# Optimization experiments

Hardware: AMD Instinct MI355X
Metric: run time of the kernel (lower is better)

## Reference

```python
import jax, jax.numpy as jnp
import numpy as np

B, C2D, C3D, H, W, N = 4, 64, 64, 256, 256, 16384
NEG_SLOPE = 0.1


def _conv1x1_lrelu(x, w, b):
    # 1x1 conv (no norm) + leaky_relu(0.1), per Conv2dNormRelu defaults
    y = jnp.einsum('bchw,oc->bohw', x, w) + b[None, :, None, None]
    return jax.nn.leaky_relu(y, NEG_SLOPE)


def _batch_gather(feat, idx):
    # feat: [B, C, N], idx: [B, P] -> [B, C, P]
    return jnp.take_along_axis(feat, idx[:, None, :], axis=2)


def setup_inputs() -> dict:
    key = jax.random.key(0)
    ks = jax.random.split(key, 14)
    f = jax.random.normal
    s = 0.05
    return {
        'xy': jax.random.uniform(ks[0], (B, 2, N), jnp.float32) * jnp.float32(W),
        'feat_2d': f(ks[1], (B, C2D, H, W), jnp.float32),
        'feat_3d': f(ks[2], (B, C3D, N), jnp.float32),
        'last_flow_2d': f(ks[3], (B, 2, H, W), jnp.float32),
        'last_flow_3d_to_2d': f(ks[4], (B, 2, N), jnp.float32),
        'nn_proj': jax.random.randint(ks[5], (B, H, W, 1), 0, N, jnp.int32),
        'w1': f(ks[6], (C3D, C3D + 5), jnp.float32) * s,
        'b1': f(ks[7], (C3D,), jnp.float32) * s,
        'w2': f(ks[8], (C3D, C3D), jnp.float32) * s,
        'b2': f(ks[9], (C3D,), jnp.float32) * s,
        'w3': f(ks[10], (C3D, C3D), jnp.float32) * s,
        'b3': f(ks[11], (C3D,), jnp.float32) * s,
        'wf': f(ks[12], (C2D, C2D + C3D), jnp.float32) * s,
        'bf': f(ks[13], (C2D,), jnp.float32) * s,
    }


def reference(xy, feat_2d, feat_3d, last_flow_2d, last_flow_3d_to_2d, nn_proj,
              w1, b1, w2, b2, w3, b3, wf, bf):
    b, _, h, w = feat_2d.shape
    # concat per-point flow onto 3D features: [B, C3D+2, N]
    feat_3d_aug = jnp.concatenate([feat_3d, last_flow_3d_to_2d], axis=1)

    idx = nn_proj[..., 0].reshape(b, h * w)  # nearest-neighbor point per pixel
    gathered = _batch_gather(feat_3d_aug, idx).reshape(b, -1, h, w)  # [B, C3D+2, H, W]
    xy_proj = _batch_gather(xy, idx).reshape(b, 2, h, w)             # [B, 2, H, W]

    # pixel-coordinate mesh grid: channel 0 = x (width), channel 1 = y (height)
    gy, gx = jnp.meshgrid(jnp.arange(h, dtype=xy.dtype), jnp.arange(w, dtype=xy.dtype), indexing='ij')
    grid = jnp.stack([gx, gy], axis=0)[None]  # [1, 2, H, W]
    offset = xy_proj - grid                    # [B, 2, H, W]

    # correlation between gathered 3D feats and 2D feats (channel mean)
    corr = jnp.mean(gathered[:, :C2D] * feat_2d, axis=1, keepdims=True)  # [B, 1, H, W]

    # last 2 channels are the projected flow; subtract detached last_flow_2d
    flow_ch = gathered[:, -2:] - jax.lax.stop_gradient(last_flow_2d)
    x = jnp.concatenate([corr, offset, gathered[:, :-2], flow_ch], axis=1)  # [B, C3D+5, H, W]

    x = _conv1x1_lrelu(x, w1, b1)
    x = _conv1x1_lrelu(x, w2, b2)
    x = _conv1x1_lrelu(x, w3, b3)
    out = _conv1x1_lrelu(jnp.concatenate([x, feat_2d], axis=1), wf, bf)  # [B, C2D, H, W]
    return out
```

## Files before the change

kernel.cpp:

```cpp
#include <hip/hip_runtime.h>

#define BB 4
#define CH 64
#define HW 65536
#define NN 16384
#define NT 128
#define TW 256
#define XPITCH 72
#define LPITCH 72
#define F2PITCH 72
#define W1OFS 0
#define W2OFS 4096
#define W3OFS 8192
#define WFOFS 12288
#define FWS_BYTE 46080
#define PTAB_BYTE 49152
#define PT_ROW 160
#define WS_NEED ((size_t)PTAB_BYTE + (size_t)BB * NN * PT_ROW)

typedef __attribute__((ext_vector_type(8))) short short8;
typedef __attribute__((ext_vector_type(4))) float f32x4;

union frag_u { unsigned short u[8]; short8 v; };
union row_u  { uint4 q[4]; unsigned short u[32]; };
union half_u { uint4 q[2]; unsigned short u[16]; };

static __device__ __forceinline__ unsigned short f2bf(float x) {
    unsigned int u = __float_as_uint(x);
    return (unsigned short)((u + 0x7fffu + ((u >> 16) & 1u)) >> 16);
}
static __device__ __forceinline__ float bf2f(unsigned short h) {
    return __uint_as_float(((unsigned int)h) << 16);
}

__global__ __launch_bounds__(256) void prep(
    const float* __restrict__ xy, const float* __restrict__ f3d,
    const float* __restrict__ lf3d,
    const float* __restrict__ w1, const float* __restrict__ b1,
    const float* __restrict__ w2, const float* __restrict__ b2,
    const float* __restrict__ w3, const float* __restrict__ b3,
    const float* __restrict__ wf, const float* __restrict__ bf,
    unsigned short* __restrict__ wpk, float* __restrict__ fws,
    char* __restrict__ pt)
{
    const int t = threadIdx.x;
    const int bx = blockIdx.x;
    if (bx >= NN / 64) {
        if (blockIdx.y != 0) return;
        const int blk = bx - NN / 64;
        if (blk == 0) {
            for (int i = t; i < 64 * 64; i += 256) {
                const int m = i >> 6, k = i & 63;
                wpk[W1OFS + i] = f2bf(w1[m * 69 + 3 + k]);
            }
        } else if (blk == 1) {
            for (int i = t; i < 64 * 64; i += 256) wpk[W2OFS + i] = f2bf(w2[i]);
        } else if (blk == 2) {
            for (int i = t; i < 64 * 64; i += 256) wpk[W3OFS + i] = f2bf(w3[i]);
        } else if (blk == 3) {
            for (int i = t; i < 64 * 128; i += 256) wpk[WFOFS + i] = f2bf(wf[i]);
        } else if (t < 64) {
            fws[t]       = b1[t];
            fws[64 + t]  = b2[t];
            fws[128 + t] = b3[t];
            fws[192 + t] = bf[t];
            fws[256 + t] = w1[t * 69 + 1];
            fws[320 + t] = w1[t * 69 + 2];
            fws[384 + t] = w1[t * 69 + 0];
            fws[448 + t] = w1[t * 69 + 67];
            fws[512 + t] = w1[t * 69 + 68];
        }
        return;
    }
    const int cq = t >> 6;
    const int l = t & 63;
    const int gn = bx * 64 + l;
    const int b = blockIdx.y;
    half_u r;
#pragma unroll
    for (int i = 0; i < 16; i++)
        r.u[i] = f2bf(f3d[(size_t)(b * CH + cq * 16 + i) * NN + gn]);
    char* row = pt + ((size_t)b * NN + gn) * PT_ROW;
    uint4* rq = (uint4*)row;
    rq[2 * cq] = r.q[0];
    rq[2 * cq + 1] = r.q[1];
    if (cq == 0) {
        float4 e;
        e.x = xy[(size_t)(b * 2 + 0) * NN + gn];
        e.y = xy[(size_t)(b * 2 + 1) * NN + gn];
        e.z = lf3d[(size_t)(b * 2 + 0) * NN + gn];
        e.w = lf3d[(size_t)(b * 2 + 1) * NN + gn];
        *(float4*)(row + 144) = e;
    }
}

struct pref_t {
    float4 fv[8];
    row_u g;
    float4 e;
    float lfx, lfy;
};

static __device__ __forceinline__ void tile_load(
    pref_t& P, const float* __restrict__ feat2d, const float* __restrict__ lf2d,
    const char* __restrict__ ptab, int b, int p_base, int w, int lane, int idx)
{
    const int ci = lane >> 3, qd = lane & 7;
    const int px0 = 32 * w + qd * 4;
#pragma unroll
    for (int cc = 0; cc < 8; cc++)
        P.fv[cc] = *(const float4*)(feat2d + (size_t)(b * CH + ci * 8 + cc) * HW + p_base + px0);
    const int cp = lane >> 5, j = lane & 31;
    const int n = 32 * w + j;
    const char* prow = ptab + ((size_t)b * NN + idx) * PT_ROW;
#pragma unroll
    for (int k = 0; k < 4; k++) P.g.q[k] = ((const uint4*)prow)[cp * 4 + k];
    if (cp == 0) {
        P.e = *(const float4*)(prow + 144);
        P.lfx = lf2d[(size_t)(b * 2 + 0) * HW + p_base + n];
        P.lfy = lf2d[(size_t)(b * 2 + 1) * HW + p_base + n];
    }
}

static __device__ __forceinline__ void tile_stage(
    const pref_t& P, unsigned short* F2, unsigned short* Xhi, int w, int lane)
{
    const int ci = lane >> 3, qd = lane & 7;
    const int px0 = 32 * w + qd * 4;
#pragma unroll
    for (int px = 0; px < 4; px++) {
        frag_u fr;
#pragma unroll
        for (int cc = 0; cc < 8; cc++)
            fr.u[cc] = f2bf(((const float*)&P.fv[cc])[px]);
        *(short8*)&F2[(px0 + px) * F2PITCH + ci * 8] = fr.v;
    }
    const int cp = lane >> 5, j = lane & 31;
    const int n = 32 * w + j;
    uint4* xp = (uint4*)&Xhi[n * XPITCH + cp * 32];
#pragma unroll
    for (int k = 0; k < 4; k++) xp[k] = P.g.q[k];
}

static __device__ __forceinline__ void tile_corr(
    const pref_t& P, const unsigned short* F2, float* offsS, float* auxS,
    int p_base, int w, int lane)
{
    const int cp = lane >> 5, j = lane & 31;
    const int n = 32 * w + j;
    const int p = p_base + n;
    frag_u f2v[4];
#pragma unroll
    for (int k = 0; k < 4; k++)
        f2v[k].v = *(const short8*)&F2[n * F2PITCH + cp * 32 + k * 8];
    float ca = 0.f;
#pragma unroll
    for (int i = 0; i < 32; i++)
        ca += bf2f(f2v[i >> 3].u[i & 7]) * bf2f(P.g.u[i]);
    ca += __shfl_xor(ca, 32);
    if (cp == 0) {
        offsS[n] = P.e.x - (float)(p & 255);
        offsS[NT + n] = P.e.y - (float)(p >> 8);
        auxS[n] = ca * (1.0f / 64.0f);
        auxS[NT + n] = P.e.z - P.lfx;
        auxS[2 * NT + n] = P.e.w - P.lfy;
    }
}

template<int KT, int KROW, bool LO>
static __device__ __forceinline__ void layer_mfma(
    const unsigned short* __restrict__ wrow,
    const unsigned short* Xh, const unsigned short* Xl,
    int w, int ln, int q, f32x4 acc[4][2])
{
#pragma unroll
    for (int kt = 0; kt < KT; kt++) {
        const int kcol = kt * 32 + q * 8;
        short8 A[4];
#pragma unroll
        for (int mi = 0; mi < 4; mi++)
            A[mi] = *(const short8*)(wrow + (mi * 16 + ln) * KROW + kcol);
#pragma unroll
        for (int ni = 0; ni < 2; ni++) {
            const int nr = 32 * w + ni * 16 + ln;
            short8 bh = *(const short8*)(Xh + nr * XPITCH + kcol);
            short8 bl = bh;
            if (LO) bl = *(const short8*)(Xl + nr * LPITCH + kcol);
#pragma unroll
            for (int mi = 0; mi < 4; mi++) {
                acc[mi][ni] = __builtin_amdgcn_mfma_f32_16x16x32_bf16(A[mi], bh, acc[mi][ni], 0, 0, 0);
                if (LO)
                    acc[mi][ni] = __builtin_amdgcn_mfma_f32_16x16x32_bf16(A[mi], bl, acc[mi][ni], 0, 0, 0);
            }
        }
    }
}

static __device__ __forceinline__ void zero_acc(f32x4 acc[4][2]) {
#pragma unroll
    for (int mi = 0; mi < 4; mi++)
#pragma unroll
        for (int ni = 0; ni < 2; ni++)
#pragma unroll
            for (int r = 0; r < 4; r++) acc[mi][ni][r] = 0.f;
}

static __device__ __forceinline__ void epi_x(
    f32x4 acc[4][2], const float* __restrict__ fws, int bofs, bool off_fix,
    const float* offsp, const float* auxp, unsigned short* Xh, unsigned short* Xl,
    int w, int ln, int q)
{
#pragma unroll
    for (int mi = 0; mi < 4; mi++) {
        const float4 bias = *(const float4*)(fws + bofs + mi * 16 + q * 4);
        float4 wox = bias, woy = bias, wco = bias, wfx = bias, wfy = bias;
        if (off_fix) {
            wox = *(const float4*)(fws + 256 + mi * 16 + q * 4);
            woy = *(const float4*)(fws + 320 + mi * 16 + q * 4);
            wco = *(const float4*)(fws + 384 + mi * 16 + q * 4);
            wfx = *(const float4*)(fws + 448 + mi * 16 + q * 4);
            wfy = *(const float4*)(fws + 512 + mi * 16 + q * 4);
        }
#pragma unroll
        for (int ni = 0; ni < 2; ni++) {
            const int nr = 32 * w + ni * 16 + ln;
            float ox = 0.f, oy = 0.f, co = 0.f, fx = 0.f, fy = 0.f;
            if (off_fix) {
                ox = offsp[nr]; oy = offsp[NT + nr];
                co = auxp[nr];  fx = auxp[NT + nr]; fy = auxp[2 * NT + nr];
            }
            unsigned int hh0 = 0, hh1 = 0, ll0 = 0, ll1 = 0;
#pragma unroll
            for (int r = 0; r < 4; r++) {
                float a = acc[mi][ni][r] + ((const float*)&bias)[r];
                if (off_fix) {
                    a += ((const float*)&wox)[r] * ox + ((const float*)&woy)[r] * oy;
                    a += ((const float*)&wco)[r] * co;
                    a += ((const float*)&wfx)[r] * fx + ((const float*)&wfy)[r] * fy;
                }
                a = fmaxf(a, 0.1f * a);
                const unsigned short hb = f2bf(a);
                const unsigned short lb = f2bf(a - bf2f(hb));
                if (r == 0) { hh0 = hb; ll0 = lb; }
                if (r == 1) { hh0 |= ((unsigned)hb) << 16; ll0 |= ((unsigned)lb) << 16; }
                if (r == 2) { hh1 = hb; ll1 = lb; }
                if (r == 3) { hh1 |= ((unsigned)hb) << 16; ll1 |= ((unsigned)lb) << 16; }
            }
            *(uint2*)&Xh[nr * XPITCH + mi * 16 + q * 4] = make_uint2(hh0, hh1);
            *(uint2*)&Xl[nr * LPITCH + mi * 16 + q * 4] = make_uint2(ll0, ll1);
        }
    }
}

static __device__ __forceinline__ void compute_tile(
    const unsigned short* Xhi, const unsigned short* Xlo, const unsigned short* F2,
    const float* offsS, const float* auxS,
    const unsigned short* __restrict__ wpk, const float* __restrict__ fws,
    float* __restrict__ out, int b, int p_base, int w, int ln, int q)
{
    f32x4 acc[4][2];
    zero_acc(acc);
    layer_mfma<2, 64, false>(wpk + W1OFS, Xhi, Xlo, w, ln, q, acc);
    epi_x(acc, fws, 0, true, offsS, auxS, (unsigned short*)Xhi, (unsigned short*)Xlo, w, ln, q);
    zero_acc(acc);
    layer_mfma<2, 64, true>(wpk + W2OFS, Xhi, Xlo, w, ln, q, acc);
    epi_x(acc, fws, 64, false, offsS, auxS, (unsigned short*)Xhi, (unsigned short*)Xlo, w, ln, q);
    zero_acc(acc);
    layer_mfma<2, 64, true>(wpk + W3OFS, Xhi, Xlo, w, ln, q, acc);
    epi_x(acc, fws, 128, false, offsS, auxS, (unsigned short*)Xhi, (unsigned short*)Xlo, w, ln, q);
    zero_acc(acc);
    layer_mfma<2, 128, true>(wpk + WFOFS, Xhi, Xlo, w, ln, q, acc);
#pragma unroll
    for (int kt = 2; kt < 4; kt++) {
        const int kcol = kt * 32 + q * 8;
        short8 A[4];
#pragma unroll
        for (int mi = 0; mi < 4; mi++)
            A[mi] = *(const short8*)(wpk + WFOFS + (mi * 16 + ln) * 128 + kcol);
#pragma unroll
        for (int ni = 0; ni < 2; ni++) {
            const int nr = 32 * w + ni * 16 + ln;
            frag_u fh;
            fh.v = *(const short8*)&F2[nr * F2PITCH + (kt - 2) * 32 + q * 8];
#pragma unroll
            for (int mi = 0; mi < 4; mi++)
                acc[mi][ni] = __builtin_amdgcn_mfma_f32_16x16x32_bf16(A[mi], fh.v, acc[mi][ni], 0, 0, 0);
        }
    }
#pragma unroll
    for (int mi = 0; mi < 4; mi++) {
        const float4 bias = *(const float4*)(fws + 192 + mi * 16 + q * 4);
#pragma unroll
        for (int ni = 0; ni < 2; ni++) {
#pragma unroll
            for (int r = 0; r < 4; r++) {
                float a = acc[mi][ni][r] + ((const float*)&bias)[r];
                a = fmaxf(a, 0.1f * a);
                const int m = mi * 16 + q * 4 + r;
                out[(size_t)(b * CH + m) * HW + p_base + 32 * w + ni * 16 + ln] = a;
            }
        }
    }
}

__global__ __launch_bounds__(256, 2) void fuse(
    const float* __restrict__ feat2d, const float* __restrict__ lf2d,
    const int* __restrict__ nn,
    const unsigned short* __restrict__ wpk, const float* __restrict__ fws,
    const char* __restrict__ ptab,
    float* __restrict__ out)
{
    __shared__ unsigned short Xhi[NT * XPITCH];
    __shared__ unsigned short Xlo[NT * LPITCH];
    __shared__ unsigned short F2[NT * F2PITCH];
    __shared__ float offsS[2 * NT];
    __shared__ float auxS[3 * NT];

    const int tid = threadIdx.x;
    const int w = tid >> 6, lane = tid & 63;
    const int q = lane >> 4, ln = lane & 15;
    const int b = blockIdx.y;
    const int p0 = blockIdx.x * TW;
    const int n = 32 * w + (lane & 31);

    const int idx0 = nn[(size_t)b * HW + p0 + n];
    const int idx1 = nn[(size_t)b * HW + p0 + NT + n];

    pref_t P0, P1;
    tile_load(P0, feat2d, lf2d, ptab, b, p0, w, lane, idx0);
    tile_stage(P0, F2, Xhi, w, lane);
    tile_load(P1, feat2d, lf2d, ptab, b, p0 + NT, w, lane, idx1);
    tile_corr(P0, F2, offsS, auxS, p0, w, lane);
    compute_tile(Xhi, Xlo, F2, offsS, auxS, wpk, fws, out, b, p0, w, ln, q);
    tile_stage(P1, F2, Xhi, w, lane);
    tile_corr(P1, F2, offsS, auxS, p0 + NT, w, lane);
    compute_tile(Xhi, Xlo, F2, offsS, auxS, wpk, fws, out, b, p0 + NT, w, ln, q);
}

__global__ __launch_bounds__(256) void fuse_slow(
    const float* __restrict__ feat2d, const float* __restrict__ lf2d,
    const float* __restrict__ xy, const float* __restrict__ feat3d,
    const float* __restrict__ lf3d, const int* __restrict__ nn,
    const float* __restrict__ w1, const float* __restrict__ b1,
    const float* __restrict__ w2, const float* __restrict__ b2,
    const float* __restrict__ w3, const float* __restrict__ b3,
    const float* __restrict__ wf, const float* __restrict__ bfv,
    float* __restrict__ out)
{
    const int p = blockIdx.x * 256 + threadIdx.x;
    const int b = blockIdx.y;
    const int idx = nn[(size_t)b * HW + p];
    const float* f3 = feat3d + (size_t)b * CH * NN + idx;
    float g[CH];
#pragma unroll
    for (int c = 0; c < CH; c++) g[c] = f3[(size_t)c * NN];
    const float fl3x = lf3d[(size_t)(b * 2 + 0) * NN + idx];
    const float fl3y = lf3d[(size_t)(b * 2 + 1) * NN + idx];
    const float xyx = xy[(size_t)(b * 2 + 0) * NN + idx];
    const float xyy = xy[(size_t)(b * 2 + 1) * NN + idx];
    const float* f2p = feat2d + (size_t)b * CH * HW + p;
    float corr = 0.f;
#pragma unroll
    for (int c = 0; c < CH; c++) corr += f2p[(size_t)c * HW] * g[c];
    corr *= (1.f / 64.f);
    float xin[69];
    xin[0] = corr;
    xin[1] = xyx - (float)(p & 255);
    xin[2] = xyy - (float)(p >> 8);
#pragma unroll
    for (int c = 0; c < CH; c++) xin[3 + c] = g[c];
    xin[67] = fl3x - lf2d[(size_t)(b * 2 + 0) * HW + p];
    xin[68] = fl3y - lf2d[(size_t)(b * 2 + 1) * HW + p];
    float x1[64], x2[64], x3[64], accv[64];
#pragma unroll
    for (int o = 0; o < 64; o++) {
        float a = b1[o];
#pragma unroll
        for (int k = 0; k < 69; k++) a += w1[o * 69 + k] * xin[k];
        x1[o] = (a >= 0.f) ? a : 0.1f * a;
    }
#pragma unroll
    for (int o = 0; o < 64; o++) {
        float a = b2[o];
#pragma unroll
        for (int k = 0; k < 64; k++) a += w2[o * 64 + k] * x1[k];
        x2[o] = (a >= 0.f) ? a : 0.1f * a;
    }
#pragma unroll
    for (int o = 0; o < 64; o++) {
        float a = b3[o];
#pragma unroll
        for (int k = 0; k < 64; k++) a += w3[o * 64 + k] * x2[k];
        x3[o] = (a >= 0.f) ? a : 0.1f * a;
    }
#pragma unroll
    for (int o = 0; o < 64; o++) {
        float a = bfv[o];
#pragma unroll
        for (int k = 0; k < 64; k++) a += wf[o * 128 + k] * x3[k];
        accv[o] = a;
    }
#pragma unroll
    for (int k = 0; k < 64; k++) {
        const float f = f2p[(size_t)k * HW];
#pragma unroll
        for (int o = 0; o < 64; o++) accv[o] += wf[o * 128 + 64 + k] * f;
    }
#pragma unroll
    for (int o = 0; o < 64; o++) {
        float a = accv[o];
        a = (a >= 0.f) ? a : 0.1f * a;
        out[(size_t)(b * CH + o) * HW + p] = a;
    }
}

extern "C" void kernel_launch(void* const* d_in, const int* in_sizes, int n_in,
                              void* d_out, int out_size, void* d_ws, size_t ws_size,
                              hipStream_t stream)
{
    const float* xy   = (const float*)d_in[0];
    const float* f2d  = (const float*)d_in[1];
    const float* f3d  = (const float*)d_in[2];
    const float* lf2d = (const float*)d_in[3];
    const float* lf3d = (const float*)d_in[4];
    const int*   nn   = (const int*)d_in[5];
    const float* w1 = (const float*)d_in[6];
    const float* b1 = (const float*)d_in[7];
    const float* w2 = (const float*)d_in[8];
    const float* b2 = (const float*)d_in[9];
    const float* w3 = (const float*)d_in[10];
    const float* b3 = (const float*)d_in[11];
    const float* wf = (const float*)d_in[12];
    const float* bf = (const float*)d_in[13];

    if (ws_size >= WS_NEED) {
        unsigned short* wpk = (unsigned short*)d_ws;
        float* fws = (float*)((char*)d_ws + FWS_BYTE);
        char* pt = (char*)d_ws + PTAB_BYTE;
        prep<<<dim3(NN / 64 + 5, BB), 256, 0, stream>>>(xy, f3d, lf3d,
                                                        w1, b1, w2, b2, w3, b3, wf, bf,
                                                        wpk, fws, pt);
        fuse<<<dim3(HW / TW, BB), 256, 0, stream>>>(f2d, lf2d, nn, wpk, fws, pt, (float*)d_out);
    } else {
        fuse_slow<<<dim3(HW / 256, BB), 256, 0, stream>>>(f2d, lf2d, xy, f3d, lf3d, nn,
                                                          w1, b1, w2, b2, w3, b3, wf, bf,
                                                          (float*)d_out);
    }
}
```

Baseline: 216.8 us.

## Keep inter-layer activations in registers via ds_bpermute instead of LDS round-trips

Layer outputs are no longer written to LDS and read back as B fragments. Each epilogue packs its hi/lo bf16 split into registers, and the next layer rebuilds the MFMA B operands with ds_bpermute lane shuffles, so the Xlo LDS buffer goes away. The change also uses the hardware v_cvt_pk_bf16_f32 instruction for packing and wraps the MFMA bursts in s_setprio. This cuts LDS traffic and footprint but adds many bpermute operations and more register pressure.

```diff
diff --git a/kernel.cpp b/kernel.cpp
--- a/kernel.cpp
+++ b/kernel.cpp
@@ -7,7 +7,6 @@
 #define NT 128
 #define TW 256
 #define XPITCH 72
-#define LPITCH 72
 #define F2PITCH 72
 #define W1OFS 0
 #define W2OFS 4096
@@ -22,6 +21,7 @@
 typedef __attribute__((ext_vector_type(4))) float f32x4;
 
 union frag_u { unsigned short u[8]; short8 v; };
+union frag2_u { unsigned short u[8]; unsigned int d[4]; short8 v; };
 union row_u  { uint4 q[4]; unsigned short u[32]; };
 union half_u { uint4 q[2]; unsigned short u[16]; };
 
@@ -31,6 +31,11 @@
 }
 static __device__ __forceinline__ float bf2f(unsigned short h) {
     return __uint_as_float(((unsigned int)h) << 16);
+}
+static __device__ __forceinline__ unsigned int cvtpk(float a, float b) {
+    unsigned int r;
+    asm("v_cvt_pk_bf16_f32 %0, %1, %2" : "=v"(r) : "v"(a), "v"(b));
+    return r;
 }
 
 __global__ __launch_bounds__(256) void prep(
@@ -129,10 +134,10 @@
     const int px0 = 32 * w + qd * 4;
 #pragma unroll
     for (int px = 0; px < 4; px++) {
-        frag_u fr;
-#pragma unroll
-        for (int cc = 0; cc < 8; cc++)
-            fr.u[cc] = f2bf(((const float*)&P.fv[cc])[px]);
+        frag2_u fr;
+#pragma unroll
+        for (int cc = 0; cc < 4; cc++)
+            fr.d[cc] = cvtpk(((const float*)&P.fv[2 * cc])[px], ((const float*)&P.fv[2 * cc + 1])[px]);
         *(short8*)&F2[(px0 + px) * F2PITCH + ci * 8] = fr.v;
     }
     const int cp = lane >> 5, j = lane & 31;
@@ -167,31 +172,63 @@
     }
 }
 
-template<int KT, int KROW, bool LO>
-static __device__ __forceinline__ void layer_mfma(
-    const unsigned short* __restrict__ wrow,
-    const unsigned short* Xh, const unsigned short* Xl,
+static __device__ __forceinline__ void layer_l1(
+    const unsigned short* __restrict__ wrow, const unsigned short* Xh,
     int w, int ln, int q, f32x4 acc[4][2])
 {
 #pragma unroll
-    for (int kt = 0; kt < KT; kt++) {
+    for (int kt = 0; kt < 2; kt++) {
         const int kcol = kt * 32 + q * 8;
         short8 A[4];
 #pragma unroll
         for (int mi = 0; mi < 4; mi++)
-            A[mi] = *(const short8*)(wrow + (mi * 16 + ln) * KROW + kcol);
+            A[mi] = *(const short8*)(wrow + (mi * 16 + ln) * 64 + kcol);
 #pragma unroll
         for (int ni = 0; ni < 2; ni++) {
             const int nr = 32 * w + ni * 16 + ln;
             short8 bh = *(const short8*)(Xh + nr * XPITCH + kcol);
-            short8 bl = bh;
-            if (LO) bl = *(const short8*)(Xl + nr * LPITCH + kcol);
+            __builtin_amdgcn_s_setprio(1);
+#pragma unroll
+            for (int mi = 0; mi < 4; mi++)
+                acc[mi][ni] = __builtin_amdgcn_mfma_f32_16x16x32_bf16(A[mi], bh, acc[mi][ni], 0, 0, 0);
+            __builtin_amdgcn_s_setprio(0);
+        }
+    }
+}
+
+template<int KROW>
+static __device__ __forceinline__ void layer_reg(
+    const unsigned short* __restrict__ wrow,
+    const unsigned int pkH[4][2][2], const unsigned int pkL[4][2][2],
+    int srcA, int srcB, int qh, int ln, int q, f32x4 acc[4][2])
+{
+#pragma unroll
+    for (int kt = 0; kt < 2; kt++) {
+        const int kcol = kt * 32 + q * 8;
+        short8 A[4];
+#pragma unroll
+        for (int mi = 0; mi < 4; mi++)
+            A[mi] = *(const short8*)(wrow + (mi * 16 + ln) * KROW + kcol);
+#pragma unroll
+        for (int ni = 0; ni < 2; ni++) {
+            frag2_u bh, bl;
+#pragma unroll
+            for (int p = 0; p < 4; p++) {
+                const int src = (p >> 1) ? srcB : srcA;
+                const unsigned h0 = (unsigned)__builtin_amdgcn_ds_bpermute(src, (int)pkH[kt * 2 + 0][ni][p & 1]);
+                const unsigned h1 = (unsigned)__builtin_amdgcn_ds_bpermute(src, (int)pkH[kt * 2 + 1][ni][p & 1]);
+                bh.d[p] = qh ? h1 : h0;
+                const unsigned l0 = (unsigned)__builtin_amdgcn_ds_bpermute(src, (int)pkL[kt * 2 + 0][ni][p & 1]);
+                const unsigned l1 = (unsigned)__builtin_amdgcn_ds_bpermute(src, (int)pkL[kt * 2 + 1][ni][p & 1]);
+                bl.d[p] = qh ? l1 : l0;
+            }
+            __builtin_amdgcn_s_setprio(1);
 #pragma unroll
             for (int mi = 0; mi < 4; mi++) {
-                acc[mi][ni] = __builtin_amdgcn_mfma_f32_16x16x32_bf16(A[mi], bh, acc[mi][ni], 0, 0, 0);
-                if (LO)
-                    acc[mi][ni] = __builtin_amdgcn_mfma_f32_16x16x32_bf16(A[mi], bl, acc[mi][ni], 0, 0, 0);
-            }
+                acc[mi][ni] = __builtin_amdgcn_mfma_f32_16x16x32_bf16(A[mi], bh.v, acc[mi][ni], 0, 0, 0);
+                acc[mi][ni] = __builtin_amdgcn_mfma_f32_16x16x32_bf16(A[mi], bl.v, acc[mi][ni], 0, 0, 0);
+            }
+            __builtin_amdgcn_s_setprio(0);
         }
     }
 }
@@ -205,9 +242,10 @@
             for (int r = 0; r < 4; r++) acc[mi][ni][r] = 0.f;
 }
 
-static __device__ __forceinline__ void epi_x(
+static __device__ __forceinline__ void epi_pack(
     f32x4 acc[4][2], const float* __restrict__ fws, int bofs, bool off_fix,
-    const float* offsp, const float* auxp, unsigned short* Xh, unsigned short* Xl,
+    const float* offsp, const float* auxp,
+    unsigned int pkH[4][2][2], unsigned int pkL[4][2][2],
     int w, int ln, int q)
 {
 #pragma unroll
@@ -229,7 +267,7 @@
                 ox = offsp[nr]; oy = offsp[NT + nr];
                 co = auxp[nr];  fx = auxp[NT + nr]; fy = auxp[2 * NT + nr];
             }
-            unsigned int hh0 = 0, hh1 = 0, ll0 = 0, ll1 = 0;
+            float av[4];
 #pragma unroll
             for (int r = 0; r < 4; r++) {
                 float a = acc[mi][ni][r] + ((const float*)&bias)[r];
@@ -238,38 +276,40 @@
                     a += ((const float*)&wco)[r] * co;
                     a += ((const float*)&wfx)[r] * fx + ((const float*)&wfy)[r] * fy;
                 }
-                a = fmaxf(a, 0.1f * a);
-                const unsigned short hb = f2bf(a);
-                const unsigned short lb = f2bf(a - bf2f(hb));
-                if (r == 0) { hh0 = hb; ll0 = lb; }
-                if (r == 1) { hh0 |= ((unsigned)hb) << 16; ll0 |= ((unsigned)lb) << 16; }
-                if (r == 2) { hh1 = hb; ll1 = lb; }
-                if (r == 3) { hh1 |= ((unsigned)hb) << 16; ll1 |= ((unsigned)lb) << 16; }
-            }
-            *(uint2*)&Xh[nr * XPITCH + mi * 16 + q * 4] = make_uint2(hh0, hh1);
-            *(uint2*)&Xl[nr * LPITCH + mi * 16 + q * 4] = make_uint2(ll0, ll1);
+                av[r] = fmaxf(a, 0.1f * a);
+            }
+#pragma unroll
+            for (int t = 0; t < 2; t++) {
+                const unsigned hh = cvtpk(av[2 * t], av[2 * t + 1]);
+                const float l0 = av[2 * t]     - __uint_as_float(hh << 16);
+                const float l1 = av[2 * t + 1] - __uint_as_float(hh & 0xffff0000u);
+                pkH[mi][ni][t] = hh;
+                pkL[mi][ni][t] = cvtpk(l0, l1);
+            }
         }
     }
 }
 
 static __device__ __forceinline__ void compute_tile(
-    const unsigned short* Xhi, const unsigned short* Xlo, const unsigned short* F2,
+    const unsigned short* Xhi, const unsigned short* F2,
     const float* offsS, const float* auxS,
     const unsigned short* __restrict__ wpk, const float* __restrict__ fws,
-    float* __restrict__ out, int b, int p_base, int w, int ln, int q)
-{
+    float* __restrict__ out, int b, int p_base, int w, int ln, int q,
+    int srcA, int srcB, int qh)
+{
+    unsigned int pkH[4][2][2], pkL[4][2][2];
     f32x4 acc[4][2];
     zero_acc(acc);
-    layer_mfma<2, 64, false>(wpk + W1OFS, Xhi, Xlo, w, ln, q, acc);
-    epi_x(acc, fws, 0, true, offsS, auxS, (unsigned short*)Xhi, (unsigned short*)Xlo, w, ln, q);
+    layer_l1(wpk + W1OFS, Xhi, w, ln, q, acc);
+    epi_pack(acc, fws, 0, true, offsS, auxS, pkH, pkL, w, ln, q);
     zero_acc(acc);
-    layer_mfma<2, 64, true>(wpk + W2OFS, Xhi, Xlo, w, ln, q, acc);
-    epi_x(acc, fws, 64, false, offsS, auxS, (unsigned short*)Xhi, (unsigned short*)Xlo, w, ln, q);
+    layer_reg<64>(wpk + W2OFS, pkH, pkL, srcA, srcB, qh, ln, q, acc);
+    epi_pack(acc, fws, 64, false, offsS, auxS, pkH, pkL, w, ln, q);
     zero_acc(acc);
-    layer_mfma<2, 64, true>(wpk + W3OFS, Xhi, Xlo, w, ln, q, acc);
-    epi_x(acc, fws, 128, false, offsS, auxS, (unsigned short*)Xhi, (unsigned short*)Xlo, w, ln, q);
+    layer_reg<64>(wpk + W3OFS, pkH, pkL, srcA, srcB, qh, ln, q, acc);
+    epi_pack(acc, fws, 128, false, offsS, auxS, pkH, pkL, w, ln, q);
     zero_acc(acc);
-    layer_mfma<2, 128, true>(wpk + WFOFS, Xhi, Xlo, w, ln, q, acc);
+    layer_reg<128>(wpk + WFOFS, pkH, pkL, srcA, srcB, qh, ln, q, acc);
 #pragma unroll
     for (int kt = 2; kt < 4; kt++) {
         const int kcol = kt * 32 + q * 8;
@@ -282,9 +322,11 @@
             const int nr = 32 * w + ni * 16 + ln;
             frag_u fh;
             fh.v = *(const short8*)&F2[nr * F2PITCH + (kt - 2) * 32 + q * 8];
+            __builtin_amdgcn_s_setprio(1);
 #pragma unroll
             for (int mi = 0; mi < 4; mi++)
                 acc[mi][ni] = __builtin_amdgcn_mfma_f32_16x16x32_bf16(A[mi], fh.v, acc[mi][ni], 0, 0, 0);
+            __builtin_amdgcn_s_setprio(0);
         }
     }
 #pragma unroll
@@ -311,7 +353,6 @@
     float* __restrict__ out)
 {
     __shared__ unsigned short Xhi[NT * XPITCH];
-    __shared__ unsigned short Xlo[NT * LPITCH];
     __shared__ unsigned short F2[NT * F2PITCH];
     __shared__ float offsS[2 * NT];
     __shared__ float auxS[3 * NT];
@@ -323,6 +364,10 @@
     const int p0 = blockIdx.x * TW;
     const int n = 32 * w + (lane & 31);
 
+    const int srcA = (((lane >> 4) & 1) * 32 + ln) * 4;
+    const int srcB = srcA + 64;
+    const int qh = q >> 1;
+
     const int idx0 = nn[(size_t)b * HW + p0 + n];
     const int idx1 = nn[(size_t)b * HW + p0 + NT + n];
 
@@ -331,10 +376,10 @@
     tile_stage(P0, F2, Xhi, w, lane);
     tile_load(P1, feat2d, lf2d, ptab, b, p0 + NT, w, lane, idx1);
     tile_corr(P0, F2, offsS, auxS, p0, w, lane);
-    compute_tile(Xhi, Xlo, F2, offsS, auxS, wpk, fws, out, b, p0, w, ln, q);
+    compute_tile(Xhi, F2, offsS, auxS, wpk, fws, out, b, p0, w, ln, q, srcA, srcB, qh);
     tile_stage(P1, F2, Xhi, w, lane);
     tile_corr(P1, F2, offsS, auxS, p0 + NT, w, lane);
-    compute_tile(Xhi, Xlo, F2, offsS, auxS, wpk, fws, out, b, p0 + NT, w, ln, q);
+    compute_tile(Xhi, F2, offsS, auxS, wpk, fws, out, b, p0 + NT, w, ln, q, srcA, srcB, qh);
 }
 
 __global__ __launch_bounds__(256) void fuse_slow(
```

Result: faster. 210.3 us (-3.0%).
